# Kernel optimization log

Measured on AMD Instinct MI355X. Metric: run time of the kernel, lower is better.

Reference implementation:

```python
import jax, jax.numpy as jnp
import numpy as np


def setup_inputs() -> dict:
    key = jax.random.key(0)
    k1, k2 = jax.random.split(key)
    B, H, S = 4, 16, 1024  # batch, heads, seq_len (attention logits [B,H,S,S])
    x = jax.random.normal(k1, (B, H, S, S), dtype=jnp.float32)
    v = jax.random.normal(k2, (B, H, 1, S), dtype=jnp.float32)  # per-key value weights
    return {"x": x, "v": v}


def reference(x, v):
    # Forward of the wrapped rule: softmax over the last (key) dim, then
    # elementwise multiplication with the value tensor (broadcast over queries).
    # The chunked vmap in the original is purely a memory-management detail of
    # its custom backward; the forward math is softmax(x) * v.
    return jax.nn.softmax(x, axis=-1) * v
```

## Files before the change

### kernel.cpp

```cpp
#include <hip/hip_runtime.h>


#define SEQ 1024
#define F4_PER_ROW (SEQ / 4)
#define WAVES_PER_BLOCK 4

__global__ __launch_bounds__(256) void softmax_mul_kernel(
    const float* __restrict__ x,
    const float* __restrict__ v,
    float* __restrict__ out,
    int rows) {
  const int wave_in_block = threadIdx.x >> 6;
  const int lane = threadIdx.x & 63;
  const int row = blockIdx.x * WAVES_PER_BLOCK + wave_in_block;
  if (row >= rows) return;

  const size_t row_off = (size_t)row * SEQ;
  const float4* __restrict__ x4 = (const float4*)(x + row_off);
  float4* __restrict__ o4 = (float4*)(out + row_off);
  const float4* __restrict__ v4 = (const float4*)(v + (size_t)(row >> 10) * SEQ);

  float4 d[4];
#pragma unroll
  for (int j = 0; j < 4; ++j) d[j] = x4[lane + 64 * j];

  float m = -INFINITY;
#pragma unroll
  for (int j = 0; j < 4; ++j)
    m = fmaxf(m, fmaxf(fmaxf(d[j].x, d[j].y), fmaxf(d[j].z, d[j].w)));
#pragma unroll
  for (int off = 32; off > 0; off >>= 1)
    m = fmaxf(m, __shfl_xor(m, off, 64));

  float s = 0.f;
#pragma unroll
  for (int j = 0; j < 4; ++j) {
    d[j].x = __expf(d[j].x - m);
    d[j].y = __expf(d[j].y - m);
    d[j].z = __expf(d[j].z - m);
    d[j].w = __expf(d[j].w - m);
    s += (d[j].x + d[j].y) + (d[j].z + d[j].w);
  }
#pragma unroll
  for (int off = 32; off > 0; off >>= 1)
    s += __shfl_xor(s, off, 64);

  const float inv = 1.0f / s;

#pragma unroll
  for (int j = 0; j < 4; ++j) {
    const float4 vv = v4[lane + 64 * j];
    float4 o;
    o.x = d[j].x * inv * vv.x;
    o.y = d[j].y * inv * vv.y;
    o.z = d[j].z * inv * vv.z;
    o.w = d[j].w * inv * vv.w;
    o4[lane + 64 * j] = o;
  }
}

extern "C" void kernel_launch(void* const* d_in, const int* in_sizes, int n_in,
                              void* d_out, int out_size, void* d_ws, size_t ws_size,
                              hipStream_t stream) {
  const float* x = (const float*)d_in[0];
  const float* v = (const float*)d_in[1];
  float* out = (float*)d_out;
  const int rows = in_sizes[0] / SEQ;
  const int grid = (rows + WAVES_PER_BLOCK - 1) / WAVES_PER_BLOCK;
  softmax_mul_kernel<<<grid, 256, 0, stream>>>(x, v, out, rows);
}
```

Before: 424.6 us.

## Process two rows per wave with nontemporal loads/stores and early v loads

Each wave now handles two consecutive rows, issuing all x loads for both rows plus the v loads up front, which gives more memory-level parallelism per wave. The x loads and output stores use nontemporal hints so the streaming data is meant to bypass cache retention. The cost is higher register use and half as many waves. It also assumes an even row count, since an odd final row would be dropped.

Result: faster. 415.6 us (-2.1%).

```diff
diff --git a/kernel.cpp b/kernel.cpp
--- a/kernel.cpp
+++ b/kernel.cpp
@@ -2,60 +2,72 @@
 
 
 #define SEQ 1024
-#define F4_PER_ROW (SEQ / 4)
 #define WAVES_PER_BLOCK 4
+
+typedef float vf4 __attribute__((ext_vector_type(4)));
 
 __global__ __launch_bounds__(256) void softmax_mul_kernel(
     const float* __restrict__ x,
     const float* __restrict__ v,
     float* __restrict__ out,
-    int rows) {
-  const int wave_in_block = threadIdx.x >> 6;
+    int npairs) {
+  const int wave = threadIdx.x >> 6;
   const int lane = threadIdx.x & 63;
-  const int row = blockIdx.x * WAVES_PER_BLOCK + wave_in_block;
-  if (row >= rows) return;
+  const int pair = blockIdx.x * WAVES_PER_BLOCK + wave;
+  if (pair >= npairs) return;
 
-  const size_t row_off = (size_t)row * SEQ;
-  const float4* __restrict__ x4 = (const float4*)(x + row_off);
-  float4* __restrict__ o4 = (float4*)(out + row_off);
-  const float4* __restrict__ v4 = (const float4*)(v + (size_t)(row >> 10) * SEQ);
+  const size_t row0 = (size_t)pair * 2;
+  const vf4* __restrict__ x4 = (const vf4*)(x + row0 * SEQ);
+  vf4* __restrict__ o4 = (vf4*)(out + row0 * SEQ);
+  const vf4* __restrict__ v4 = (const vf4*)(v + (row0 >> 10) * SEQ);
 
-  float4 d[4];
+  vf4 a[4], b[4], vv[4];
 #pragma unroll
-  for (int j = 0; j < 4; ++j) d[j] = x4[lane + 64 * j];
+  for (int j = 0; j < 4; ++j) a[j] = __builtin_nontemporal_load(&x4[lane + 64 * j]);
+#pragma unroll
+  for (int j = 0; j < 4; ++j) b[j] = __builtin_nontemporal_load(&x4[256 + lane + 64 * j]);
+#pragma unroll
+  for (int j = 0; j < 4; ++j) vv[j] = v4[lane + 64 * j];
 
-  float m = -INFINITY;
-#pragma unroll
-  for (int j = 0; j < 4; ++j)
-    m = fmaxf(m, fmaxf(fmaxf(d[j].x, d[j].y), fmaxf(d[j].z, d[j].w)));
-#pragma unroll
-  for (int off = 32; off > 0; off >>= 1)
-    m = fmaxf(m, __shfl_xor(m, off, 64));
-
-  float s = 0.f;
+  float ma = -INFINITY, mb = -INFINITY;
 #pragma unroll
   for (int j = 0; j < 4; ++j) {
-    d[j].x = __expf(d[j].x - m);
-    d[j].y = __expf(d[j].y - m);
-    d[j].z = __expf(d[j].z - m);
-    d[j].w = __expf(d[j].w - m);
-    s += (d[j].x + d[j].y) + (d[j].z + d[j].w);
+    ma = fmaxf(ma, fmaxf(fmaxf(a[j].x, a[j].y), fmaxf(a[j].z, a[j].w)));
+    mb = fmaxf(mb, fmaxf(fmaxf(b[j].x, b[j].y), fmaxf(b[j].z, b[j].w)));
   }
 #pragma unroll
-  for (int off = 32; off > 0; off >>= 1)
-    s += __shfl_xor(s, off, 64);
+  for (int off = 32; off > 0; off >>= 1) {
+    ma = fmaxf(ma, __shfl_xor(ma, off, 64));
+    mb = fmaxf(mb, __shfl_xor(mb, off, 64));
+  }
 
-  const float inv = 1.0f / s;
+  float sa = 0.f, sb = 0.f;
+#pragma unroll
+  for (int j = 0; j < 4; ++j) {
+    a[j].x = __expf(a[j].x - ma); a[j].y = __expf(a[j].y - ma);
+    a[j].z = __expf(a[j].z - ma); a[j].w = __expf(a[j].w - ma);
+    b[j].x = __expf(b[j].x - mb); b[j].y = __expf(b[j].y - mb);
+    b[j].z = __expf(b[j].z - mb); b[j].w = __expf(b[j].w - mb);
+    sa += (a[j].x + a[j].y) + (a[j].z + a[j].w);
+    sb += (b[j].x + b[j].y) + (b[j].z + b[j].w);
+  }
+#pragma unroll
+  for (int off = 32; off > 0; off >>= 1) {
+    sa += __shfl_xor(sa, off, 64);
+    sb += __shfl_xor(sb, off, 64);
+  }
+  const float ia = 1.0f / sa;
+  const float ib = 1.0f / sb;
 
 #pragma unroll
   for (int j = 0; j < 4; ++j) {
-    const float4 vv = v4[lane + 64 * j];
-    float4 o;
-    o.x = d[j].x * inv * vv.x;
-    o.y = d[j].y * inv * vv.y;
-    o.z = d[j].z * inv * vv.z;
-    o.w = d[j].w * inv * vv.w;
-    o4[lane + 64 * j] = o;
+    vf4 oa, ob;
+    oa.x = a[j].x * ia * vv[j].x; oa.y = a[j].y * ia * vv[j].y;
+    oa.z = a[j].z * ia * vv[j].z; oa.w = a[j].w * ia * vv[j].w;
+    ob.x = b[j].x * ib * vv[j].x; ob.y = b[j].y * ib * vv[j].y;
+    ob.z = b[j].z * ib * vv[j].z; ob.w = b[j].w * ib * vv[j].w;
+    __builtin_nontemporal_store(oa, &o4[lane + 64 * j]);
+    __builtin_nontemporal_store(ob, &o4[256 + lane + 64 * j]);
   }
 }
 
@@ -66,6 +78,7 @@
   const float* v = (const float*)d_in[1];
   float* out = (float*)d_out;
   const int rows = in_sizes[0] / SEQ;
-  const int grid = (rows + WAVES_PER_BLOCK - 1) / WAVES_PER_BLOCK;
-  softmax_mul_kernel<<<grid, 256, 0, stream>>>(x, v, out, rows);
+  const int npairs = rows / 2;
+  const int grid = (npairs + WAVES_PER_BLOCK - 1) / WAVES_PER_BLOCK;
+  softmax_mul_kernel<<<grid, 256, 0, stream>>>(x, v, out, npairs);
 }
```
